# Performance work log

Hardware: AMD Instinct MI355X
Metric: run time of the kernel (lower is better)

## Reference

```python
import jax, jax.numpy as jnp
import numpy as np

VOCAB = 50257
DIM = 1024
B, S = 8, 2048


def setup_inputs() -> dict:
    key = jax.random.key(0)
    k1, k2, k3 = jax.random.split(key, 3)
    x = jax.random.randint(k1, (B, S), 0, VOCAB, dtype=jnp.int32)
    # int8 quantized embedding table, stored as int8 like the torch buffer
    weights = jax.random.randint(k2, (VOCAB, DIM), -128, 127, dtype=jnp.int32).astype(jnp.int8)
    # per-row dequantization scales (shape [num_embeddings]; quantize() computes per-row)
    scales = jax.random.normal(k3, (VOCAB,), dtype=jnp.float32)
    return {"x": x, "weights": weights, "scales": scales}


def reference(x, weights, scales):
    # Faithful to torch forward: dequantize the ENTIRE table (cast + per-row
    # scale multiply), then embedding gather.
    converted = weights.astype(jnp.float32) * scales[:, None]  # [VOCAB, DIM]
    return converted[x]  # [B, S, DIM]
```

## Files before the change

kernel.cpp:

```cpp
#include <hip/hip_runtime.h>
#include <stdint.h>


__global__ void qe_k(const int* __restrict__ x, const int* __restrict__ w,
                     const float* __restrict__ scales, float* __restrict__ out) {
    const int token = blockIdx.x, t = threadIdx.x;

    const int4 p = *reinterpret_cast<const int4*>(w);
    const bool wide =
        (p.x == (int)(int8_t)p.x) && (p.y == (int)(int8_t)p.y) &&
        (p.z == (int)(int8_t)p.z) && (p.w == (int)(int8_t)p.w);

    const int idx = x[token];
    const float s = scales[idx];

    float4 o;
    if (wide) {
        const int4 v = reinterpret_cast<const int4*>(w + (size_t)idx * 1024)[t];
        o.x = (float)v.x * s;
        o.y = (float)v.y * s;
        o.z = (float)v.z * s;
        o.w = (float)v.w * s;
    } else {
        const int r = reinterpret_cast<const int*>(
            reinterpret_cast<const int8_t*>(w) + (size_t)idx * 1024)[t];
        o.x = (float)(int8_t)(r)       * s;
        o.y = (float)(int8_t)(r >> 8)  * s;
        o.z = (float)(int8_t)(r >> 16) * s;
        o.w = (float)(int8_t)(r >> 24) * s;
    }

    reinterpret_cast<float4*>(out + (size_t)token * 1024)[t] = o;
}

extern "C" void kernel_launch(void* const* d_in, const int* in_sizes, int n_in,
                              void* d_out, int out_size, void* d_ws, size_t ws_size,
                              hipStream_t stream) {
    const int n_tokens = out_size / 1024;
    if (n_tokens <= 0) return;

    int iw = 0;
    for (int i = 1; i < n_in; ++i)
        if (in_sizes[i] > in_sizes[iw]) iw = i;
    int ix = -1, is = -1;
    for (int i = 0; i < n_in; ++i) {
        if (i == iw) continue;
        if (in_sizes[i] == n_tokens && ix < 0) ix = i; else is = i;
    }
    if (ix < 0) ix = (iw == 0) ? 1 : 0;
    if (is < 0) is = 3 - ix - iw;

    qe_k<<<n_tokens, 256, 0, stream>>>((const int*)d_in[ix], (const int*)d_in[iw],
                                       (const float*)d_in[is], (float*)d_out);
}
```

Measured before the change: 25.80 us.

## Use grid-stride persistent blocks with index prefetch and nontemporal output stores

Caps the grid at 2048 blocks and has each block loop over tokens grid-stride, loading the next token's index one step ahead. Output is written with nontemporal stores so the 64MB float result bypasses cache retention. This cuts block launch overhead and keeps the large write stream from polluting cache, at the cost of less parallelism per block and a serial dependency inside the loop.

```diff
diff --git a/kernel.cpp b/kernel.cpp
--- a/kernel.cpp
+++ b/kernel.cpp
@@ -2,35 +2,50 @@
 #include <stdint.h>
 
 
-__global__ void qe_k(const int* __restrict__ x, const int* __restrict__ w,
-                     const float* __restrict__ scales, float* __restrict__ out) {
-    const int token = blockIdx.x, t = threadIdx.x;
+typedef float f32x4 __attribute__((ext_vector_type(4)));
+
+__global__ __launch_bounds__(256) void qe_k(const int* __restrict__ x,
+                                            const int* __restrict__ w,
+                                            const float* __restrict__ scales,
+                                            float* __restrict__ out,
+                                            int n_tokens) {
+    const int t = threadIdx.x;
 
     const int4 p = *reinterpret_cast<const int4*>(w);
     const bool wide =
         (p.x == (int)(int8_t)p.x) && (p.y == (int)(int8_t)p.y) &&
         (p.z == (int)(int8_t)p.z) && (p.w == (int)(int8_t)p.w);
 
-    const int idx = x[token];
-    const float s = scales[idx];
+    int token = blockIdx.x;
+    int idx   = (token < n_tokens) ? x[token] : 0;
 
-    float4 o;
-    if (wide) {
-        const int4 v = reinterpret_cast<const int4*>(w + (size_t)idx * 1024)[t];
-        o.x = (float)v.x * s;
-        o.y = (float)v.y * s;
-        o.z = (float)v.z * s;
-        o.w = (float)v.w * s;
-    } else {
-        const int r = reinterpret_cast<const int*>(
-            reinterpret_cast<const int8_t*>(w) + (size_t)idx * 1024)[t];
-        o.x = (float)(int8_t)(r)       * s;
-        o.y = (float)(int8_t)(r >> 8)  * s;
-        o.z = (float)(int8_t)(r >> 16) * s;
-        o.w = (float)(int8_t)(r >> 24) * s;
+    while (token < n_tokens) {
+        const int next_token = token + gridDim.x;
+        const int next_idx   = (next_token < n_tokens) ? x[next_token] : 0;
+
+        const float s = scales[idx];
+        f32x4 o;
+        if (wide) {
+            const int4 v = reinterpret_cast<const int4*>(w + (size_t)idx * 1024)[t];
+            o.x = (float)v.x * s;
+            o.y = (float)v.y * s;
+            o.z = (float)v.z * s;
+            o.w = (float)v.w * s;
+        } else {
+            const int r = reinterpret_cast<const int*>(
+                reinterpret_cast<const int8_t*>(w) + (size_t)idx * 1024)[t];
+            o.x = (float)(int8_t)(r)       * s;
+            o.y = (float)(int8_t)(r >> 8)  * s;
+            o.z = (float)(int8_t)(r >> 16) * s;
+            o.w = (float)(int8_t)(r >> 24) * s;
+        }
+
+        __builtin_nontemporal_store(
+            o, reinterpret_cast<f32x4*>(out + (size_t)token * 1024) + t);
+
+        token = next_token;
+        idx   = next_idx;
     }
-
-    reinterpret_cast<float4*>(out + (size_t)token * 1024)[t] = o;
 }
 
 extern "C" void kernel_launch(void* const* d_in, const int* in_sizes, int n_in,
@@ -50,6 +65,8 @@
     if (ix < 0) ix = (iw == 0) ? 1 : 0;
     if (is < 0) is = 3 - ix - iw;
 
-    qe_k<<<n_tokens, 256, 0, stream>>>((const int*)d_in[ix], (const int*)d_in[iw],
-                                       (const float*)d_in[is], (float*)d_out);
+    const int blocks = (n_tokens < 2048) ? n_tokens : 2048;
+    qe_k<<<blocks, 256, 0, stream>>>((const int*)d_in[ix], (const int*)d_in[iw],
+                                     (const float*)d_in[is], (float*)d_out,
+                                     n_tokens);
 }
```

Measured after the change: 26.57 us. +3.0%, slower.
